# Optimization experiments

Measured on AMD Instinct MI355X. Metric: run time of the kernel, lower is better.

## Reference

```python
import jax, jax.numpy as jnp
import numpy as np

N_NODES = 50000


def gcn_conv(x, W, b, src, dst, n):
    # dense transform first (as PyG GCNConv does), then sparse aggregate
    h = x @ W  # [N, out]
    # add self loops
    loop = jnp.arange(n, dtype=src.dtype)
    s = jnp.concatenate([src, loop])
    d = jnp.concatenate([dst, loop])
    # symmetric normalization: deg over targets with unit edge weights
    deg = jax.ops.segment_sum(jnp.ones_like(d, dtype=h.dtype), d, num_segments=n)
    dinv = jnp.where(deg > 0, jax.lax.rsqrt(deg), 0.0)
    norm = dinv[s] * dinv[d]  # [E+N]
    msg = h[s] * norm[:, None]  # gather + scale
    out = jax.ops.segment_sum(msg, d, num_segments=n)  # scatter-add
    return out + b


def setup_inputs() -> dict:
    key = jax.random.key(0)
    k1, k2, k3, k4, k5 = jax.random.split(key, 5)
    in_dim, hid, out_dim = 256, 128, 16
    x = jax.random.normal(k1, (N_NODES, in_dim), dtype=jnp.float32)
    edge_index = jax.random.randint(k2, (2, 800000), 0, N_NODES, dtype=jnp.int64)
    # Glorot-style init for GCNConv weights, zero bias (PyG default)
    W1 = jax.random.normal(k3, (in_dim, hid), dtype=jnp.float32) / np.sqrt(in_dim)
    b1 = jnp.zeros((hid,), dtype=jnp.float32)
    W2 = jax.random.normal(k4, (hid, out_dim), dtype=jnp.float32) / np.sqrt(hid)
    b2 = jnp.zeros((out_dim,), dtype=jnp.float32)
    return {"x": x, "edge_index": edge_index, "W1": W1, "b1": b1, "W2": W2, "b2": b2}


def reference(x, edge_index, W1, b1, W2, b2):
    # eval-mode forward: dropout is identity
    src, dst = edge_index[0], edge_index[1]
    n = x.shape[0]
    h = gcn_conv(x, W1, b1, src, dst, n)
    h = jax.nn.relu(h)
    h = gcn_conv(h, W2, b2, src, dst, n)
    return jax.nn.log_softmax(h, axis=1)
```

## Files before the change

### kernel.cpp

```cpp
#include <hip/hip_runtime.h>
#include <hip/hip_bf16.h>

#define N_NODES 50000
#define E_EDGES 800000
#define IN_DIM  256
#define HID     128
#define OUT_DIM 16

#define NBUCK 391
#define NBLK  128
#define P2CAP 4096
#define GB1   391

using frag_ab = __attribute__((ext_vector_type(8))) short;
using frag_cd = __attribute__((ext_vector_type(4))) float;

static __device__ inline short f2bf(float f) {
    union { float f; unsigned u; } v; v.f = f;
    unsigned r = (v.u + 0x7fffu + ((v.u >> 16) & 1u)) >> 16;
    return (short)r;
}
static __device__ inline float bflo(unsigned u) {
    union { unsigned u; float f; } v; v.u = u << 16; return v.f;
}
static __device__ inline float bfhi(unsigned u) {
    union { unsigned u; float f; } v; v.u = u & 0xffff0000u; return v.f;
}
static __device__ inline unsigned packbf(float a, float b) {
    return (unsigned)(unsigned short)f2bf(a) | ((unsigned)(unsigned short)f2bf(b) << 16);
}

__global__ __launch_bounds__(512) void k1_gemm1_csra(const float* __restrict__ x,
                                                     const float* __restrict__ W1,
                                                     const int4* __restrict__ dst4,
                                                     const float* __restrict__ W2,
                                                     int* __restrict__ cnt_bb,
                                                     short* __restrict__ w2t,
                                                     short* __restrict__ h1s) {
    __shared__ uint4 lwt[64 * 64];
    int tid = threadIdx.x;

    if (blockIdx.x == GB1 + NBLK) {
        int n0 = tid >> 5, k0 = (tid & 31) * 4;
#pragma unroll
        for (int i = 0; i < 4; ++i)
            w2t[n0 * HID + k0 + i] = f2bf(W2[(k0 + i) * OUT_DIM + n0]);
        return;
    }
    if (blockIdx.x >= GB1) {
        int* hist = (int*)lwt;
        int bb = blockIdx.x - GB1;
        for (int i = tid; i < NBUCK; i += 512) hist[i] = 0;
        __syncthreads();
        for (int i = bb * 512 + tid; i < E_EDGES / 4; i += NBLK * 512) {
            int4 d = dst4[i];
            atomicAdd(&hist[d.x >> 7], 1);
            atomicAdd(&hist[d.y >> 7], 1);
            atomicAdd(&hist[d.z >> 7], 1);
            atomicAdd(&hist[d.w >> 7], 1);
        }
        __syncthreads();
        for (int i = tid; i < NBUCK; i += 512) cnt_bb[i * NBLK + bb] = hist[i];
        return;
    }

#pragma unroll
    for (int it = 0; it < 8; ++it) {
        int j = it * 512 + tid;
        int f = j >> 6, lane_ = j & 63;
        int kt = f >> 3, tt = f & 7;
        int mm = lane_ & 15, qq = lane_ >> 4;
        int c = tt * 16 + mm;
        int k0 = kt * 32 + qq * 8;
        unsigned p[4];
#pragma unroll
        for (int i = 0; i < 4; ++i)
            p[i] = packbf(W1[(k0 + 2 * i) * HID + c], W1[(k0 + 2 * i + 1) * HID + c]);
        uint4 v; v.x = p[0]; v.y = p[1]; v.z = p[2]; v.w = p[3];
        lwt[j] = v;
    }

    int wave = tid >> 6;
    int lane = tid & 63;
    int m = lane & 15;
    int q = lane >> 4;
    int row0 = blockIdx.x * 128 + wave * 16;
    int arow_idx = row0 + m;
    const float4* arow4 = (const float4*)(x + (size_t)(arow_idx < N_NODES ? arow_idx : 0) * IN_DIM);

    frag_ab a[8];
#pragma unroll
    for (int kt = 0; kt < 8; ++kt) {
        float4 f0 = arow4[kt * 8 + q * 2];
        float4 f1 = arow4[kt * 8 + q * 2 + 1];
        a[kt][0] = f2bf(f0.x); a[kt][1] = f2bf(f0.y); a[kt][2] = f2bf(f0.z); a[kt][3] = f2bf(f0.w);
        a[kt][4] = f2bf(f1.x); a[kt][5] = f2bf(f1.y); a[kt][6] = f2bf(f1.z); a[kt][7] = f2bf(f1.w);
    }

    frag_cd acc[8];
#pragma unroll
    for (int t = 0; t < 8; ++t) acc[t] = frag_cd{0.f, 0.f, 0.f, 0.f};

    __syncthreads();

#pragma unroll
    for (int kt = 0; kt < 8; ++kt) {
#pragma unroll
        for (int t = 0; t < 8; ++t) {
            frag_ab b = *(const frag_ab*)&lwt[(kt * 8 + t) * 64 + lane];
            acc[t] = __builtin_amdgcn_mfma_f32_16x16x32_bf16(a[kt], b, acc[t], 0, 0, 0);
        }
    }

#pragma unroll
    for (int t = 0; t < 8; ++t) {
#pragma unroll
        for (int r = 0; r < 4; ++r) {
            int orow = row0 + q * 4 + r;
            if (orow < N_NODES)
                h1s[(size_t)orow * HID + t * 16 + m] = f2bf(acc[t][r]);
        }
    }
}

__global__ __launch_bounds__(NBLK) void csr_b1(int* __restrict__ cnt_bb,
                                               int* __restrict__ btot) {
    __shared__ int sm[NBLK];
    int b = blockIdx.x, t = threadIdx.x;
    int v = cnt_bb[b * NBLK + t];
    sm[t] = v;
    __syncthreads();
    for (int o = 1; o < NBLK; o <<= 1) {
        int u = (t >= o) ? sm[t - o] : 0;
        __syncthreads();
        sm[t] += u;
        __syncthreads();
    }
    cnt_bb[b * NBLK + t] = sm[t] - v;
    if (t == NBLK - 1) btot[b] = sm[t];
}

__global__ __launch_bounds__(512) void csr_c2(const int4* __restrict__ src4,
                                              const int4* __restrict__ dst4,
                                              const int* __restrict__ cnt_bb,
                                              const int* __restrict__ btot,
                                              int* __restrict__ bbase,
                                              unsigned* __restrict__ tmp) {
    __shared__ int run[NBUCK];
    __shared__ int sc[512];
    int t = threadIdx.x;
    int v = (t < NBUCK) ? btot[t] : 0;
    sc[t] = v;
    __syncthreads();
    for (int o = 1; o < 512; o <<= 1) {
        int u = (t >= o) ? sc[t - o] : 0;
        __syncthreads();
        sc[t] += u;
        __syncthreads();
    }
    if (t < NBUCK) {
        int exc = sc[t] - v;
        run[t] = exc + cnt_bb[t * NBLK + blockIdx.x];
        if (blockIdx.x == 0) bbase[t] = exc;
    }
    if (blockIdx.x == 0 && t == 511) bbase[NBUCK] = sc[511];
    __syncthreads();
    for (int i = blockIdx.x * 512 + t; i < E_EDGES / 4; i += NBLK * 512) {
        int4 d = dst4[i];
        int4 s = src4[i];
        int p0 = atomicAdd(&run[d.x >> 7], 1);
        tmp[p0] = (unsigned)s.x | ((unsigned)(d.x & 127) << 17);
        int p1 = atomicAdd(&run[d.y >> 7], 1);
        tmp[p1] = (unsigned)s.y | ((unsigned)(d.y & 127) << 17);
        int p2 = atomicAdd(&run[d.z >> 7], 1);
        tmp[p2] = (unsigned)s.z | ((unsigned)(d.z & 127) << 17);
        int p3 = atomicAdd(&run[d.w >> 7], 1);
        tmp[p3] = (unsigned)s.w | ((unsigned)(d.w & 127) << 17);
    }
}

__global__ __launch_bounds__(256) void csr_p2s(const unsigned* __restrict__ tmp,
                                               const int* __restrict__ bbase,
                                               int* __restrict__ rowptr,
                                               float* __restrict__ dinv,
                                               int* __restrict__ ssrc,
                                               short* __restrict__ h1s) {
    __shared__ unsigned ed[P2CAP];
    __shared__ int cnt[128];
    __shared__ int off[128];
    __shared__ float sdv[128];
    int b = blockIdx.x, t = threadIdx.x;
    int base = bbase[b];
    int m = bbase[b + 1] - base;
    if (m > P2CAP) m = P2CAP;
    if (t < 128) cnt[t] = 0;
    __syncthreads();
    for (int i = t; i < m; i += 256) {
        unsigned v = tmp[base + i];
        ed[i] = v;
        atomicAdd(&cnt[v >> 17], 1);
    }
    __syncthreads();
    if (t < 128) off[t] = cnt[t];
    __syncthreads();
    for (int o = 1; o < 128; o <<= 1) {
        int u = (t >= o && t < 128) ? off[t - o] : 0;
        __syncthreads();
        if (t < 128) off[t] += u;
        __syncthreads();
    }
    if (t < 128) {
        int node = b * 128 + t;
        int ex = off[t] - cnt[t];
        float dv = rsqrtf((float)(cnt[t] + 1));
        sdv[t] = dv;
        if (node < N_NODES) {
            rowptr[node] = base + ex;
            dinv[node] = dv;
        }
        off[t] = ex;
    }
    if (b == NBUCK - 1 && t == 0) rowptr[N_NODES] = E_EDGES;
    __syncthreads();
    for (int i = t; i < m; i += 256) {
        unsigned v = ed[i];
        int p = atomicAdd(&off[v >> 17], 1);
        ssrc[base + p] = (int)(v & 0x1FFFF);
    }
    for (int idx = t; idx < 128 * 16; idx += 256) {
        int nl = idx >> 4;
        int wd = idx & 15;
        int node = b * 128 + nl;
        if (node < N_NODES) {
            uint4* p = (uint4*)(h1s + (size_t)node * HID) + wd;
            uint4 u = *p;
            float dv = sdv[nl];
            u.x = packbf(dv * bflo(u.x), dv * bfhi(u.x));
            u.y = packbf(dv * bflo(u.y), dv * bfhi(u.y));
            u.z = packbf(dv * bflo(u.z), dv * bfhi(u.z));
            u.w = packbf(dv * bflo(u.w), dv * bfhi(u.w));
            *p = u;
        }
    }
}

__global__ __launch_bounds__(256) void agg1_pull(const short* __restrict__ h1s,
                                                 const float* __restrict__ dinv,
                                                 const float* __restrict__ b1,
                                                 const int* __restrict__ rowptr,
                                                 const int* __restrict__ ssrc,
                                                 uint4* __restrict__ out1) {
    int wave = threadIdx.x >> 6;
    int lane = threadIdx.x & 63;
    int node = __builtin_amdgcn_readfirstlane(blockIdx.x * 4 + wave);
    if (node >= N_NODES) return;
    int eo = lane >> 4;
    int g  = lane & 15;

    int lo = rowptr[node], hi = rowptr[node + 1];
    float dd = dinv[node];
    float a0 = 0.f, a1 = 0.f, a2 = 0.f, a3 = 0.f;
    float a4 = 0.f, a5 = 0.f, a6 = 0.f, a7 = 0.f;

    if (eo == 0) {
        uint4 u = *(const uint4*)(h1s + (size_t)node * HID + g * 8);
        a0 = bflo(u.x); a1 = bfhi(u.x); a2 = bflo(u.y); a3 = bfhi(u.y);
        a4 = bflo(u.z); a5 = bfhi(u.z); a6 = bflo(u.w); a7 = bfhi(u.w);
    }

    int e = lo;
    for (; e + 16 <= hi; e += 16) {
        int s0 = ssrc[e + eo];
        int s1 = ssrc[e + 4 + eo];
        int s2 = ssrc[e + 8 + eo];
        int s3 = ssrc[e + 12 + eo];
        uint4 u0 = *(const uint4*)(h1s + (size_t)s0 * HID + g * 8);
        uint4 u1 = *(const uint4*)(h1s + (size_t)s1 * HID + g * 8);
        uint4 u2 = *(const uint4*)(h1s + (size_t)s2 * HID + g * 8);
        uint4 u3 = *(const uint4*)(h1s + (size_t)s3 * HID + g * 8);
        a0 += bflo(u0.x); a1 += bfhi(u0.x); a2 += bflo(u0.y); a3 += bfhi(u0.y);
        a4 += bflo(u0.z); a5 += bfhi(u0.z); a6 += bflo(u0.w); a7 += bfhi(u0.w);
        a0 += bflo(u1.x); a1 += bfhi(u1.x); a2 += bflo(u1.y); a3 += bfhi(u1.y);
        a4 += bflo(u1.z); a5 += bfhi(u1.z); a6 += bflo(u1.w); a7 += bfhi(u1.w);
        a0 += bflo(u2.x); a1 += bfhi(u2.x); a2 += bflo(u2.y); a3 += bfhi(u2.y);
        a4 += bflo(u2.z); a5 += bfhi(u2.z); a6 += bflo(u2.w); a7 += bfhi(u2.w);
        a0 += bflo(u3.x); a1 += bfhi(u3.x); a2 += bflo(u3.y); a3 += bfhi(u3.y);
        a4 += bflo(u3.z); a5 += bfhi(u3.z); a6 += bflo(u3.w); a7 += bfhi(u3.w);
    }
    for (; e + 4 <= hi; e += 4) {
        int s = ssrc[e + eo];
        uint4 u = *(const uint4*)(h1s + (size_t)s * HID + g * 8);
        a0 += bflo(u.x); a1 += bfhi(u.x); a2 += bflo(u.y); a3 += bfhi(u.y);
        a4 += bflo(u.z); a5 += bfhi(u.z); a6 += bflo(u.w); a7 += bfhi(u.w);
    }
    if (eo < hi - e) {
        int s = ssrc[e + eo];
        uint4 u = *(const uint4*)(h1s + (size_t)s * HID + g * 8);
        a0 += bflo(u.x); a1 += bfhi(u.x); a2 += bflo(u.y); a3 += bfhi(u.y);
        a4 += bflo(u.z); a5 += bfhi(u.z); a6 += bflo(u.w); a7 += bfhi(u.w);
    }

    a0 += __shfl_xor(a0, 16); a1 += __shfl_xor(a1, 16);
    a2 += __shfl_xor(a2, 16); a3 += __shfl_xor(a3, 16);
    a4 += __shfl_xor(a4, 16); a5 += __shfl_xor(a5, 16);
    a6 += __shfl_xor(a6, 16); a7 += __shfl_xor(a7, 16);
    a0 += __shfl_xor(a0, 32); a1 += __shfl_xor(a1, 32);
    a2 += __shfl_xor(a2, 32); a3 += __shfl_xor(a3, 32);
    a4 += __shfl_xor(a4, 32); a5 += __shfl_xor(a5, 32);
    a6 += __shfl_xor(a6, 32); a7 += __shfl_xor(a7, 32);

    if (eo == 0) {
        float4 bA = *(const float4*)(b1 + g * 8);
        float4 bB = *(const float4*)(b1 + g * 8 + 4);
        float o0 = fmaxf(fmaf(dd, a0, bA.x), 0.f);
        float o1 = fmaxf(fmaf(dd, a1, bA.y), 0.f);
        float o2 = fmaxf(fmaf(dd, a2, bA.z), 0.f);
        float o3 = fmaxf(fmaf(dd, a3, bA.w), 0.f);
        float o4 = fmaxf(fmaf(dd, a4, bB.x), 0.f);
        float o5 = fmaxf(fmaf(dd, a5, bB.y), 0.f);
        float o6 = fmaxf(fmaf(dd, a6, bB.z), 0.f);
        float o7 = fmaxf(fmaf(dd, a7, bB.w), 0.f);
        uint4 st;
        st.x = packbf(o0, o1); st.y = packbf(o2, o3);
        st.z = packbf(o4, o5); st.w = packbf(o6, o7);
        out1[(size_t)node * 16 + g] = st;
    }
}

__global__ __launch_bounds__(256) void gemm2_mfma(const short* __restrict__ out1,
                                                  const short* __restrict__ w2t,
                                                  const float* __restrict__ dinv,
                                                  short* __restrict__ h2s) {
    int wave = threadIdx.x >> 6;
    int lane = threadIdx.x & 63;
    int m = lane & 15;
    int q = lane >> 4;
    int row0 = blockIdx.x * 64 + wave * 16;
    int arow = row0 + m;
    if (arow >= N_NODES) arow = N_NODES - 1;
    const short* ap = out1 + (size_t)arow * HID + q * 8;
    const short* bp = w2t + m * HID + q * 8;

    frag_cd acc = frag_cd{0.f, 0.f, 0.f, 0.f};
#pragma unroll
    for (int kt = 0; kt < 4; ++kt) {
        frag_ab a = *(const frag_ab*)(ap + kt * 32);
        frag_ab b = *(const frag_ab*)(bp + kt * 32);
        acc = __builtin_amdgcn_mfma_f32_16x16x32_bf16(a, b, acc, 0, 0, 0);
    }
#pragma unroll
    for (int r = 0; r < 4; ++r) {
        int row = row0 + q * 4 + r;
        if (row < N_NODES)
            h2s[(size_t)row * OUT_DIM + m] = f2bf(acc[r] * dinv[row]);
    }
}

__global__ __launch_bounds__(256) void agg2_pull(const unsigned* __restrict__ h2s,
                                                 const float* __restrict__ dinv,
                                                 const float* __restrict__ b2,
                                                 const int* __restrict__ rowptr,
                                                 const int* __restrict__ ssrc,
                                                 float* __restrict__ out) {
    int wave = threadIdx.x >> 6;
    int lane = threadIdx.x & 63;
    int node = __builtin_amdgcn_readfirstlane(blockIdx.x * 4 + wave);
    if (node >= N_NODES) return;
    int eo = lane >> 3;
    int g  = lane & 7;

    int lo = rowptr[node], hi = rowptr[node + 1];
    float a0 = 0.f, a1 = 0.f;
    if (eo == 0) {
        unsigned u = h2s[(size_t)node * 8 + g];
        a0 = bflo(u); a1 = bfhi(u);
    }
    int e = lo;
    for (; e + 16 <= hi; e += 16) {
        int s0 = ssrc[e + eo];
        int s1 = ssrc[e + 8 + eo];
        unsigned u0 = h2s[(size_t)s0 * 8 + g];
        unsigned u1 = h2s[(size_t)s1 * 8 + g];
        a0 += bflo(u0); a1 += bfhi(u0);
        a0 += bflo(u1); a1 += bfhi(u1);
    }
    for (; e + 8 <= hi; e += 8) {
        int s = ssrc[e + eo];
        unsigned u = h2s[(size_t)s * 8 + g];
        a0 += bflo(u); a1 += bfhi(u);
    }
    if (eo < hi - e) {
        int s = ssrc[e + eo];
        unsigned u = h2s[(size_t)s * 8 + g];
        a0 += bflo(u); a1 += bfhi(u);
    }

    a0 += __shfl_xor(a0, 8);  a1 += __shfl_xor(a1, 8);
    a0 += __shfl_xor(a0, 16); a1 += __shfl_xor(a1, 16);
    a0 += __shfl_xor(a0, 32); a1 += __shfl_xor(a1, 32);

    float dd = dinv[node];
    float2 bb = *(const float2*)(b2 + 2 * g);
    float v0 = fmaf(dd, a0, bb.x);
    float v1 = fmaf(dd, a1, bb.y);

    float m = fmaxf(v0, v1);
#pragma unroll
    for (int msk = 1; msk < 8; msk <<= 1) m = fmaxf(m, __shfl_xor(m, msk));
    float s2 = __expf(v0 - m) + __expf(v1 - m);
#pragma unroll
    for (int msk = 1; msk < 8; msk <<= 1) s2 += __shfl_xor(s2, msk);
    float lse = m + __logf(s2);
    if (eo == 0) {
        float2 o; o.x = v0 - lse; o.y = v1 - lse;
        *(float2*)(out + (size_t)node * OUT_DIM + 2 * g) = o;
    }
}

extern "C" void kernel_launch(void* const* d_in, const int* in_sizes, int n_in,
                              void* d_out, int out_size, void* d_ws, size_t ws_size,
                              hipStream_t stream) {
    const float* x  = (const float*)d_in[0];
    const int*   ei = (const int*)d_in[1];
    const float* W1 = (const float*)d_in[2];
    const float* b1 = (const float*)d_in[3];
    const float* W2 = (const float*)d_in[4];
    const float* b2 = (const float*)d_in[5];
    float* out = (float*)d_out;

    const int n = N_NODES;
    const int e = E_EDGES;
    const int* srcp = ei;
    const int* dstp = ei + e;

    char* w = (char*)d_ws;
    int*      cnt_bb = (int*)w;        w += (size_t)NBUCK * NBLK * 4;
    int*      btot   = (int*)w;        w += (size_t)NBUCK * 4;
    int*      bbase  = (int*)w;        w += (size_t)(NBUCK + 1) * 4;
    int*      rowptr = (int*)w;        w += (size_t)(n + 1) * 4;
    float*    dinv   = (float*)w;      w += (size_t)n * 4;
    unsigned* tmp    = (unsigned*)w;   w += (size_t)e * 4;
    int*      ssrc   = (int*)w;        w += (size_t)e * 4;
    short*    w2t    = (short*)w;      w += (size_t)OUT_DIM * HID * 2;
    short*    h1s    = (short*)w;      w += (size_t)n * HID * 2;
    short*    out1   = (short*)w;      w += (size_t)n * HID * 2;
    short*    h2s    = (short*)w;      w += (size_t)n * OUT_DIM * 2;

    auto blk = [](long long total, int b) { return (int)((total + b - 1) / b); };

    k1_gemm1_csra<<<GB1 + NBLK + 1, 512, 0, stream>>>(x, W1, (const int4*)dstp, W2,
                                                      cnt_bb, w2t, h1s);
    csr_b1<<<NBUCK, NBLK, 0, stream>>>(cnt_bb, btot);
    csr_c2<<<NBLK, 512, 0, stream>>>((const int4*)srcp, (const int4*)dstp,
                                     cnt_bb, btot, bbase, tmp);
    csr_p2s<<<NBUCK, 256, 0, stream>>>(tmp, bbase, rowptr, dinv, ssrc, h1s);
    agg1_pull<<<blk(n, 4), 256, 0, stream>>>(h1s, dinv, b1, rowptr, ssrc, (uint4*)out1);
    gemm2_mfma<<<blk(n, 64), 256, 0, stream>>>(out1, w2t, dinv, h2s);
    agg2_pull<<<blk(n, 4), 256, 0, stream>>>((const unsigned*)h2s, dinv, b2,
                                             rowptr, ssrc, out);
}
```

Before: 189.6 us.

## Fuse layer-2 GEMM into aggregation and merge bucket scan into scatter kernel

The separate csr_b1 scan kernel is removed. Each csr_c2b block now computes its per-bucket totals and prefix directly from cnt_bb rows. The agg1 kernel now multiplies the ReLU'd aggregated row by W2 in fp32 using shuffles, so out1 is never written and gemm2 is gone. This drops two launches and an N×128 bf16 round trip to memory. In exchange, each csr block redundantly reads the whole cnt_bb matrix, and agg1 does extra FMA and shuffle work per node.

New measurement: 213.4 us. +12.6%, slower.

```diff
diff --git a/kernel.cpp b/kernel.cpp
--- a/kernel.cpp
+++ b/kernel.cpp
@@ -33,20 +33,11 @@
 __global__ __launch_bounds__(512) void k1_gemm1_csra(const float* __restrict__ x,
                                                      const float* __restrict__ W1,
                                                      const int4* __restrict__ dst4,
-                                                     const float* __restrict__ W2,
                                                      int* __restrict__ cnt_bb,
-                                                     short* __restrict__ w2t,
                                                      short* __restrict__ h1s) {
     __shared__ uint4 lwt[64 * 64];
     int tid = threadIdx.x;
 
-    if (blockIdx.x == GB1 + NBLK) {
-        int n0 = tid >> 5, k0 = (tid & 31) * 4;
-#pragma unroll
-        for (int i = 0; i < 4; ++i)
-            w2t[n0 * HID + k0 + i] = f2bf(W2[(k0 + i) * OUT_DIM + n0]);
-        return;
-    }
     if (blockIdx.x >= GB1) {
         int* hist = (int*)lwt;
         int bb = blockIdx.x - GB1;
@@ -123,34 +114,28 @@
     }
 }
 
-__global__ __launch_bounds__(NBLK) void csr_b1(int* __restrict__ cnt_bb,
-                                               int* __restrict__ btot) {
-    __shared__ int sm[NBLK];
-    int b = blockIdx.x, t = threadIdx.x;
-    int v = cnt_bb[b * NBLK + t];
-    sm[t] = v;
-    __syncthreads();
-    for (int o = 1; o < NBLK; o <<= 1) {
-        int u = (t >= o) ? sm[t - o] : 0;
-        __syncthreads();
-        sm[t] += u;
-        __syncthreads();
-    }
-    cnt_bb[b * NBLK + t] = sm[t] - v;
-    if (t == NBLK - 1) btot[b] = sm[t];
-}
-
-__global__ __launch_bounds__(512) void csr_c2(const int4* __restrict__ src4,
-                                              const int4* __restrict__ dst4,
-                                              const int* __restrict__ cnt_bb,
-                                              const int* __restrict__ btot,
-                                              int* __restrict__ bbase,
-                                              unsigned* __restrict__ tmp) {
+__global__ __launch_bounds__(512) void csr_c2b(const int4* __restrict__ src4,
+                                               const int4* __restrict__ dst4,
+                                               const int* __restrict__ cnt_bb,
+                                               int* __restrict__ bbase,
+                                               unsigned* __restrict__ tmp) {
     __shared__ int run[NBUCK];
     __shared__ int sc[512];
     int t = threadIdx.x;
-    int v = (t < NBUCK) ? btot[t] : 0;
-    sc[t] = v;
+    int j = blockIdx.x;
+    int tot = 0, pre = 0;
+    if (t < NBUCK) {
+        const int4* row = (const int4*)(cnt_bb + t * NBLK);
+#pragma unroll 4
+        for (int b4 = 0; b4 < NBLK / 4; ++b4) {
+            int4 c = row[b4];
+            int b = b4 * 4;
+            tot += c.x + c.y + c.z + c.w;
+            pre += (b + 0 < j ? c.x : 0) + (b + 1 < j ? c.y : 0)
+                 + (b + 2 < j ? c.z : 0) + (b + 3 < j ? c.w : 0);
+        }
+    }
+    sc[t] = tot;
     __syncthreads();
     for (int o = 1; o < 512; o <<= 1) {
         int u = (t >= o) ? sc[t - o] : 0;
@@ -159,13 +144,13 @@
         __syncthreads();
     }
     if (t < NBUCK) {
-        int exc = sc[t] - v;
-        run[t] = exc + cnt_bb[t * NBLK + blockIdx.x];
-        if (blockIdx.x == 0) bbase[t] = exc;
-    }
-    if (blockIdx.x == 0 && t == 511) bbase[NBUCK] = sc[511];
-    __syncthreads();
-    for (int i = blockIdx.x * 512 + t; i < E_EDGES / 4; i += NBLK * 512) {
+        int exc = sc[t] - tot;
+        run[t] = exc + pre;
+        if (j == 0) bbase[t] = exc;
+    }
+    if (j == 0 && t == 511) bbase[NBUCK] = sc[511];
+    __syncthreads();
+    for (int i = j * 512 + t; i < E_EDGES / 4; i += NBLK * 512) {
         int4 d = dst4[i];
         int4 s = src4[i];
         int p0 = atomicAdd(&run[d.x >> 7], 1);
@@ -244,12 +229,13 @@
     }
 }
 
-__global__ __launch_bounds__(256) void agg1_pull(const short* __restrict__ h1s,
-                                                 const float* __restrict__ dinv,
-                                                 const float* __restrict__ b1,
-                                                 const int* __restrict__ rowptr,
-                                                 const int* __restrict__ ssrc,
-                                                 uint4* __restrict__ out1) {
+__global__ __launch_bounds__(256) void agg1_w2(const short* __restrict__ h1s,
+                                               const float* __restrict__ dinv,
+                                               const float* __restrict__ b1,
+                                               const float* __restrict__ W2,
+                                               const int* __restrict__ rowptr,
+                                               const int* __restrict__ ssrc,
+                                               short* __restrict__ h2s) {
     int wave = threadIdx.x >> 6;
     int lane = threadIdx.x & 63;
     int node = __builtin_amdgcn_readfirstlane(blockIdx.x * 4 + wave);
@@ -309,50 +295,37 @@
     a4 += __shfl_xor(a4, 32); a5 += __shfl_xor(a5, 32);
     a6 += __shfl_xor(a6, 32); a7 += __shfl_xor(a7, 32);
 
-    if (eo == 0) {
-        float4 bA = *(const float4*)(b1 + g * 8);
-        float4 bB = *(const float4*)(b1 + g * 8 + 4);
-        float o0 = fmaxf(fmaf(dd, a0, bA.x), 0.f);
-        float o1 = fmaxf(fmaf(dd, a1, bA.y), 0.f);
-        float o2 = fmaxf(fmaf(dd, a2, bA.z), 0.f);
-        float o3 = fmaxf(fmaf(dd, a3, bA.w), 0.f);
-        float o4 = fmaxf(fmaf(dd, a4, bB.x), 0.f);
-        float o5 = fmaxf(fmaf(dd, a5, bB.y), 0.f);
-        float o6 = fmaxf(fmaf(dd, a6, bB.z), 0.f);
-        float o7 = fmaxf(fmaf(dd, a7, bB.w), 0.f);
-        uint4 st;
-        st.x = packbf(o0, o1); st.y = packbf(o2, o3);
-        st.z = packbf(o4, o5); st.w = packbf(o6, o7);
-        out1[(size_t)node * 16 + g] = st;
-    }
-}
-
-__global__ __launch_bounds__(256) void gemm2_mfma(const short* __restrict__ out1,
-                                                  const short* __restrict__ w2t,
-                                                  const float* __restrict__ dinv,
-                                                  short* __restrict__ h2s) {
-    int wave = threadIdx.x >> 6;
-    int lane = threadIdx.x & 63;
-    int m = lane & 15;
-    int q = lane >> 4;
-    int row0 = blockIdx.x * 64 + wave * 16;
-    int arow = row0 + m;
-    if (arow >= N_NODES) arow = N_NODES - 1;
-    const short* ap = out1 + (size_t)arow * HID + q * 8;
-    const short* bp = w2t + m * HID + q * 8;
-
-    frag_cd acc = frag_cd{0.f, 0.f, 0.f, 0.f};
-#pragma unroll
-    for (int kt = 0; kt < 4; ++kt) {
-        frag_ab a = *(const frag_ab*)(ap + kt * 32);
-        frag_ab b = *(const frag_ab*)(bp + kt * 32);
-        acc = __builtin_amdgcn_mfma_f32_16x16x32_bf16(a, b, acc, 0, 0, 0);
-    }
-#pragma unroll
-    for (int r = 0; r < 4; ++r) {
-        int row = row0 + q * 4 + r;
-        if (row < N_NODES)
-            h2s[(size_t)row * OUT_DIM + m] = f2bf(acc[r] * dinv[row]);
+    float4 bA = *(const float4*)(b1 + g * 8);
+    float4 bB = *(const float4*)(b1 + g * 8 + 4);
+    float vv[8];
+    vv[0] = fmaxf(fmaf(dd, a0, bA.x), 0.f);
+    vv[1] = fmaxf(fmaf(dd, a1, bA.y), 0.f);
+    vv[2] = fmaxf(fmaf(dd, a2, bA.z), 0.f);
+    vv[3] = fmaxf(fmaf(dd, a3, bA.w), 0.f);
+    vv[4] = fmaxf(fmaf(dd, a4, bB.x), 0.f);
+    vv[5] = fmaxf(fmaf(dd, a5, bB.y), 0.f);
+    vv[6] = fmaxf(fmaf(dd, a6, bB.z), 0.f);
+    vv[7] = fmaxf(fmaf(dd, a7, bB.w), 0.f);
+
+    float p0 = 0.f, p1 = 0.f, p2 = 0.f, p3 = 0.f;
+#pragma unroll
+    for (int i = 0; i < 8; ++i) {
+        float4 w2r = *(const float4*)(W2 + (g * 8 + i) * OUT_DIM + eo * 4);
+        p0 = fmaf(vv[i], w2r.x, p0);
+        p1 = fmaf(vv[i], w2r.y, p1);
+        p2 = fmaf(vv[i], w2r.z, p2);
+        p3 = fmaf(vv[i], w2r.w, p3);
+    }
+#pragma unroll
+    for (int msk = 1; msk <= 8; msk <<= 1) {
+        p0 += __shfl_xor(p0, msk); p1 += __shfl_xor(p1, msk);
+        p2 += __shfl_xor(p2, msk); p3 += __shfl_xor(p3, msk);
+    }
+    if (g == 0) {
+        uint2 st;
+        st.x = packbf(p0 * dd, p1 * dd);
+        st.y = packbf(p2 * dd, p3 * dd);
+        *(uint2*)(h2s + (size_t)node * OUT_DIM + eo * 4) = st;
     }
 }
 
@@ -435,27 +408,21 @@
 
     char* w = (char*)d_ws;
     int*      cnt_bb = (int*)w;        w += (size_t)NBUCK * NBLK * 4;
-    int*      btot   = (int*)w;        w += (size_t)NBUCK * 4;
     int*      bbase  = (int*)w;        w += (size_t)(NBUCK + 1) * 4;
     int*      rowptr = (int*)w;        w += (size_t)(n + 1) * 4;
     float*    dinv   = (float*)w;      w += (size_t)n * 4;
     unsigned* tmp    = (unsigned*)w;   w += (size_t)e * 4;
     int*      ssrc   = (int*)w;        w += (size_t)e * 4;
-    short*    w2t    = (short*)w;      w += (size_t)OUT_DIM * HID * 2;
     short*    h1s    = (short*)w;      w += (size_t)n * HID * 2;
-    short*    out1   = (short*)w;      w += (size_t)n * HID * 2;
     short*    h2s    = (short*)w;      w += (size_t)n * OUT_DIM * 2;
 
     auto blk = [](long long total, int b) { return (int)((total + b - 1) / b); };
 
-    k1_gemm1_csra<<<GB1 + NBLK + 1, 512, 0, stream>>>(x, W1, (const int4*)dstp, W2,
-                                                      cnt_bb, w2t, h1s);
-    csr_b1<<<NBUCK, NBLK, 0, stream>>>(cnt_bb, btot);
-    csr_c2<<<NBLK, 512, 0, stream>>>((const int4*)srcp, (const int4*)dstp,
-                                     cnt_bb, btot, bbase, tmp);
+    k1_gemm1_csra<<<GB1 + NBLK, 512, 0, stream>>>(x, W1, (const int4*)dstp, cnt_bb, h1s);
+    csr_c2b<<<NBLK, 512, 0, stream>>>((const int4*)srcp, (const int4*)dstp,
+                                      cnt_bb, bbase, tmp);
     csr_p2s<<<NBUCK, 256, 0, stream>>>(tmp, bbase, rowptr, dinv, ssrc, h1s);
-    agg1_pull<<<blk(n, 4), 256, 0, stream>>>(h1s, dinv, b1, rowptr, ssrc, (uint4*)out1);
-    gemm2_mfma<<<blk(n, 64), 256, 0, stream>>>(out1, w2t, dinv, h2s);
+    agg1_w2<<<blk(n, 4), 256, 0, stream>>>(h1s, dinv, b1, W2, rowptr, ssrc, h2s);
     agg2_pull<<<blk(n, 4), 256, 0, stream>>>((const unsigned*)h2s, dinv, b2,
                                              rowptr, ssrc, out);
 }
```

## Fold degree normalization into GEMM1 epilogue via early global degree histogram

Applied to the files above, without the earlier changes.

Computes per-node in-degree with global atomics in a new first kernel alongside the bucket histogram. GEMM1 then applies the rsqrt-degree scale in its epilogue and writes dinv, so the separate read-modify-write pass over h1s in the CSR sort kernel is removed. The bucket prefix-scan is merged into the GEMM launch, dropping one kernel. The cost is 800k global atomics, an extra memset, and the GEMM no longer overlapping with the histogram in a single launch.

New measurement: 222.7 us. 1.17x slower.

```diff
diff --git a/kernel.cpp b/kernel.cpp
--- a/kernel.cpp
+++ b/kernel.cpp
@@ -30,37 +30,62 @@
     return (unsigned)(unsigned short)f2bf(a) | ((unsigned)(unsigned short)f2bf(b) << 16);
 }
 
-__global__ __launch_bounds__(512) void k1_gemm1_csra(const float* __restrict__ x,
-                                                     const float* __restrict__ W1,
-                                                     const int4* __restrict__ dst4,
-                                                     const float* __restrict__ W2,
-                                                     int* __restrict__ cnt_bb,
-                                                     short* __restrict__ w2t,
-                                                     short* __restrict__ h1s) {
-    __shared__ uint4 lwt[64 * 64];
+__global__ __launch_bounds__(512) void k1_csra_deg(const int4* __restrict__ dst4,
+                                                   const float* __restrict__ W2,
+                                                   int* __restrict__ cnt_bb,
+                                                   int* __restrict__ deg,
+                                                   short* __restrict__ w2t) {
     int tid = threadIdx.x;
-
-    if (blockIdx.x == GB1 + NBLK) {
+    if (blockIdx.x == NBLK) {
         int n0 = tid >> 5, k0 = (tid & 31) * 4;
 #pragma unroll
         for (int i = 0; i < 4; ++i)
             w2t[n0 * HID + k0 + i] = f2bf(W2[(k0 + i) * OUT_DIM + n0]);
         return;
     }
+    __shared__ int hist[NBUCK];
+    int bb = blockIdx.x;
+    for (int i = tid; i < NBUCK; i += 512) hist[i] = 0;
+    __syncthreads();
+    for (int i = bb * 512 + tid; i < E_EDGES / 4; i += NBLK * 512) {
+        int4 d = dst4[i];
+        atomicAdd(&hist[d.x >> 7], 1);
+        atomicAdd(&hist[d.y >> 7], 1);
+        atomicAdd(&hist[d.z >> 7], 1);
+        atomicAdd(&hist[d.w >> 7], 1);
+        atomicAdd(&deg[d.x], 1);
+        atomicAdd(&deg[d.y], 1);
+        atomicAdd(&deg[d.z], 1);
+        atomicAdd(&deg[d.w], 1);
+    }
+    __syncthreads();
+    for (int i = tid; i < NBUCK; i += 512) cnt_bb[i * NBLK + bb] = hist[i];
+}
+
+__global__ __launch_bounds__(512) void k2_gemm1_b1(const float* __restrict__ x,
+                                                   const float* __restrict__ W1,
+                                                   const int* __restrict__ deg,
+                                                   int* __restrict__ cnt_bb,
+                                                   int* __restrict__ btot,
+                                                   float* __restrict__ dinv,
+                                                   short* __restrict__ h1s) {
+    __shared__ uint4 lwt[64 * 64];
+    int tid = threadIdx.x;
+
     if (blockIdx.x >= GB1) {
-        int* hist = (int*)lwt;
-        int bb = blockIdx.x - GB1;
-        for (int i = tid; i < NBUCK; i += 512) hist[i] = 0;
+        int* sm = (int*)lwt;
+        int b = blockIdx.x - GB1, t = tid;
+        int v = 0;
+        if (t < NBLK) { v = cnt_bb[b * NBLK + t]; sm[t] = v; }
         __syncthreads();
-        for (int i = bb * 512 + tid; i < E_EDGES / 4; i += NBLK * 512) {
-            int4 d = dst4[i];
-            atomicAdd(&hist[d.x >> 7], 1);
-            atomicAdd(&hist[d.y >> 7], 1);
-            atomicAdd(&hist[d.z >> 7], 1);
-            atomicAdd(&hist[d.w >> 7], 1);
+        for (int o = 1; o < NBLK; o <<= 1) {
+            int u = (t >= o && t < NBLK) ? sm[t - o] : 0;
+            __syncthreads();
+            if (t < NBLK) sm[t] += u;
+            __syncthreads();
         }
-        __syncthreads();
-        for (int i = tid; i < NBUCK; i += 512) cnt_bb[i * NBLK + bb] = hist[i];
+        if (t < NBLK) cnt_bb[b * NBLK + t] = sm[t] - v;
+        if (t == NBLK - 1) btot[b] = sm[t];
         return;
     }
 
@@ -112,32 +137,28 @@
         }
     }
 
+    float dv[4];
+#pragma unroll
+    for (int r = 0; r < 4; ++r) {
+        int orow = row0 + q * 4 + r;
+        dv[r] = (orow < N_NODES) ? rsqrtf((float)(deg[orow] + 1)) : 0.f;
+    }
+    if (m == 0) {
+#pragma unroll
+        for (int r = 0; r < 4; ++r) {
+            int orow = row0 + q * 4 + r;
+            if (orow < N_NODES) dinv[orow] = dv[r];
+        }
+    }
 #pragma unroll
     for (int t = 0; t < 8; ++t) {
 #pragma unroll
         for (int r = 0; r < 4; ++r) {
             int orow = row0 + q * 4 + r;
             if (orow < N_NODES)
-                h1s[(size_t)orow * HID + t * 16 + m] = f2bf(acc[t][r]);
+                h1s[(size_t)orow * HID + t * 16 + m] = f2bf(acc[t][r] * dv[r]);
         }
     }
-}
-
-__global__ __launch_bounds__(NBLK) void csr_b1(int* __restrict__ cnt_bb,
-                                               int* __restrict__ btot) {
-    __shared__ int sm[NBLK];
-    int b = blockIdx.x, t = threadIdx.x;
-    int v = cnt_bb[b * NBLK + t];
-    sm[t] = v;
-    __syncthreads();
-    for (int o = 1; o < NBLK; o <<= 1) {
-        int u = (t >= o) ? sm[t - o] : 0;
-        __syncthreads();
-        sm[t] += u;
-        __syncthreads();
-    }
-    cnt_bb[b * NBLK + t] = sm[t] - v;
-    if (t == NBLK - 1) btot[b] = sm[t];
 }
 
 __global__ __launch_bounds__(512) void csr_c2(const int4* __restrict__ src4,
@@ -179,16 +200,13 @@
     }
 }
 
-__global__ __launch_bounds__(256) void csr_p2s(const unsigned* __restrict__ tmp,
-                                               const int* __restrict__ bbase,
-                                               int* __restrict__ rowptr,
-                                               float* __restrict__ dinv,
-                                               int* __restrict__ ssrc,
-                                               short* __restrict__ h1s) {
+__global__ __launch_bounds__(256) void csr_p2(const unsigned* __restrict__ tmp,
+                                              const int* __restrict__ bbase,
+                                              int* __restrict__ rowptr,
+                                              int* __restrict__ ssrc) {
     __shared__ unsigned ed[P2CAP];
     __shared__ int cnt[128];
     __shared__ int off[128];
-    __shared__ float sdv[128];
     int b = blockIdx.x, t = threadIdx.x;
     int base = bbase[b];
     int m = bbase[b + 1] - base;
@@ -212,12 +230,7 @@
     if (t < 128) {
         int node = b * 128 + t;
         int ex = off[t] - cnt[t];
-        float dv = rsqrtf((float)(cnt[t] + 1));
-        sdv[t] = dv;
-        if (node < N_NODES) {
-            rowptr[node] = base + ex;
-            dinv[node] = dv;
-        }
+        if (node < N_NODES) rowptr[node] = base + ex;
         off[t] = ex;
     }
     if (b == NBUCK - 1 && t == 0) rowptr[N_NODES] = E_EDGES;
@@ -226,21 +239,6 @@
         unsigned v = ed[i];
         int p = atomicAdd(&off[v >> 17], 1);
         ssrc[base + p] = (int)(v & 0x1FFFF);
-    }
-    for (int idx = t; idx < 128 * 16; idx += 256) {
-        int nl = idx >> 4;
-        int wd = idx & 15;
-        int node = b * 128 + nl;
-        if (node < N_NODES) {
-            uint4* p = (uint4*)(h1s + (size_t)node * HID) + wd;
-            uint4 u = *p;
-            float dv = sdv[nl];
-            u.x = packbf(dv * bflo(u.x), dv * bfhi(u.x));
-            u.y = packbf(dv * bflo(u.y), dv * bfhi(u.y));
-            u.z = packbf(dv * bflo(u.z), dv * bfhi(u.z));
-            u.w = packbf(dv * bflo(u.w), dv * bfhi(u.w));
-            *p = u;
-        }
     }
 }
 
@@ -437,6 +435,7 @@
     int*      cnt_bb = (int*)w;        w += (size_t)NBUCK * NBLK * 4;
     int*      btot   = (int*)w;        w += (size_t)NBUCK * 4;
     int*      bbase  = (int*)w;        w += (size_t)(NBUCK + 1) * 4;
+    int*      deg    = (int*)w;        w += (size_t)n * 4;
     int*      rowptr = (int*)w;        w += (size_t)(n + 1) * 4;
     float*    dinv   = (float*)w;      w += (size_t)n * 4;
     unsigned* tmp    = (unsigned*)w;   w += (size_t)e * 4;
@@ -448,12 +447,12 @@
 
     auto blk = [](long long total, int b) { return (int)((total + b - 1) / b); };
 
-    k1_gemm1_csra<<<GB1 + NBLK + 1, 512, 0, stream>>>(x, W1, (const int4*)dstp, W2,
-                                                      cnt_bb, w2t, h1s);
-    csr_b1<<<NBUCK, NBLK, 0, stream>>>(cnt_bb, btot);
+    hipMemsetAsync(deg, 0, (size_t)n * sizeof(int), stream);
+    k1_csra_deg<<<NBLK + 1, 512, 0, stream>>>((const int4*)dstp, W2, cnt_bb, deg, w2t);
+    k2_gemm1_b1<<<GB1 + NBUCK, 512, 0, stream>>>(x, W1, deg, cnt_bb, btot, dinv, h1s);
     csr_c2<<<NBLK, 512, 0, stream>>>((const int4*)srcp, (const int4*)dstp,
                                      cnt_bb, btot, bbase, tmp);
-    csr_p2s<<<NBUCK, 256, 0, stream>>>(tmp, bbase, rowptr, dinv, ssrc, h1s);
+    csr_p2<<<NBUCK, 256, 0, stream>>>(tmp, bbase, rowptr, ssrc);
     agg1_pull<<<blk(n, 4), 256, 0, stream>>>(h1s, dinv, b1, rowptr, ssrc, (uint4*)out1);
     gemm2_mfma<<<blk(n, 64), 256, 0, stream>>>(out1, w2t, dinv, h2s);
     agg2_pull<<<blk(n, 4), 256, 0, stream>>>((const unsigned*)h2s, dinv, b2,
```

## Fold bucket prefix scan into scatter kernel and move degree scaling earlier

Applied to the files above, without the earlier changes.

Removes the separate per-bucket scan kernel: each scatter block now recomputes bucket totals and its own prefix directly from the count matrix. Node degrees are counted with global atomics during the histogram pass, so dinv and the h1 prescaling can run in extra blocks of the scatter kernel instead of in the final CSR pass. This drops one kernel launch and takes the scaling pass off the critical tail. In exchange it adds 800K global atomics, a memset, and redundant reads of the count matrix in every scatter block.

Measured after the change: 217.1 us. 14.5% more time.

```diff
diff --git a/kernel.cpp b/kernel.cpp
--- a/kernel.cpp
+++ b/kernel.cpp
@@ -11,6 +11,7 @@
 #define NBLK  128
 #define P2CAP 4096
 #define GB1   391
+#define NCHUNK 98
 
 using frag_ab = __attribute__((ext_vector_type(8))) short;
 using frag_cd = __attribute__((ext_vector_type(4))) float;
@@ -35,6 +36,7 @@
                                                      const int4* __restrict__ dst4,
                                                      const float* __restrict__ W2,
                                                      int* __restrict__ cnt_bb,
+                                                     int* __restrict__ deg,
                                                      short* __restrict__ w2t,
                                                      short* __restrict__ h1s) {
     __shared__ uint4 lwt[64 * 64];
@@ -58,6 +60,10 @@
             atomicAdd(&hist[d.y >> 7], 1);
             atomicAdd(&hist[d.z >> 7], 1);
             atomicAdd(&hist[d.w >> 7], 1);
+            atomicAdd(&deg[d.x], 1);
+            atomicAdd(&deg[d.y], 1);
+            atomicAdd(&deg[d.z], 1);
+            atomicAdd(&deg[d.w], 1);
         }
         __syncthreads();
         for (int i = tid; i < NBUCK; i += 512) cnt_bb[i * NBLK + bb] = hist[i];
@@ -123,34 +129,51 @@
     }
 }
 
-__global__ __launch_bounds__(NBLK) void csr_b1(int* __restrict__ cnt_bb,
-                                               int* __restrict__ btot) {
-    __shared__ int sm[NBLK];
-    int b = blockIdx.x, t = threadIdx.x;
-    int v = cnt_bb[b * NBLK + t];
-    sm[t] = v;
-    __syncthreads();
-    for (int o = 1; o < NBLK; o <<= 1) {
-        int u = (t >= o) ? sm[t - o] : 0;
-        __syncthreads();
-        sm[t] += u;
-        __syncthreads();
-    }
-    cnt_bb[b * NBLK + t] = sm[t] - v;
-    if (t == NBLK - 1) btot[b] = sm[t];
-}
-
-__global__ __launch_bounds__(512) void csr_c2(const int4* __restrict__ src4,
-                                              const int4* __restrict__ dst4,
-                                              const int* __restrict__ cnt_bb,
-                                              const int* __restrict__ btot,
-                                              int* __restrict__ bbase,
-                                              unsigned* __restrict__ tmp) {
+__global__ __launch_bounds__(512) void k2_scatter_scale(const int4* __restrict__ src4,
+                                                        const int4* __restrict__ dst4,
+                                                        const int* __restrict__ cnt_bb,
+                                                        const int* __restrict__ deg,
+                                                        int* __restrict__ bbase,
+                                                        float* __restrict__ dinv,
+                                                        short* __restrict__ h1s,
+                                                        unsigned* __restrict__ tmp) {
+    int t = threadIdx.x;
+    if (blockIdx.x >= NBLK) {
+        int base_node = (blockIdx.x - NBLK) * 512;
+        for (int idx = t; idx < 512 * 16; idx += 512) {
+            int nl = idx >> 4;
+            int wd = idx & 15;
+            int node = base_node + nl;
+            if (node < N_NODES) {
+                float dv = rsqrtf((float)(deg[node] + 1));
+                if (wd == 0) dinv[node] = dv;
+                uint4* p = (uint4*)(h1s + (size_t)node * HID) + wd;
+                uint4 u = *p;
+                u.x = packbf(dv * bflo(u.x), dv * bfhi(u.x));
+                u.y = packbf(dv * bflo(u.y), dv * bfhi(u.y));
+                u.z = packbf(dv * bflo(u.z), dv * bfhi(u.z));
+                u.w = packbf(dv * bflo(u.w), dv * bfhi(u.w));
+                *p = u;
+            }
+        }
+        return;
+    }
     __shared__ int run[NBUCK];
     __shared__ int sc[512];
-    int t = threadIdx.x;
-    int v = (t < NBUCK) ? btot[t] : 0;
-    sc[t] = v;
+    int j = blockIdx.x;
+    int tot = 0, pre = 0;
+    if (t < NBUCK) {
+        const int4* row = (const int4*)(cnt_bb + t * NBLK);
+#pragma unroll 4
+        for (int b4 = 0; b4 < NBLK / 4; ++b4) {
+            int4 c = row[b4];
+            int b = b4 * 4;
+            tot += c.x + c.y + c.z + c.w;
+            pre += (b + 0 < j ? c.x : 0) + (b + 1 < j ? c.y : 0)
+                 + (b + 2 < j ? c.z : 0) + (b + 3 < j ? c.w : 0);
+        }
+    }
+    sc[t] = tot;
     __syncthreads();
     for (int o = 1; o < 512; o <<= 1) {
         int u = (t >= o) ? sc[t - o] : 0;
@@ -159,13 +182,13 @@
         __syncthreads();
     }
     if (t < NBUCK) {
-        int exc = sc[t] - v;
-        run[t] = exc + cnt_bb[t * NBLK + blockIdx.x];
-        if (blockIdx.x == 0) bbase[t] = exc;
-    }
-    if (blockIdx.x == 0 && t == 511) bbase[NBUCK] = sc[511];
-    __syncthreads();
-    for (int i = blockIdx.x * 512 + t; i < E_EDGES / 4; i += NBLK * 512) {
+        int exc = sc[t] - tot;
+        run[t] = exc + pre;
+        if (j == 0) bbase[t] = exc;
+    }
+    if (j == 0 && t == 511) bbase[NBUCK] = sc[511];
+    __syncthreads();
+    for (int i = j * 512 + t; i < E_EDGES / 4; i += NBLK * 512) {
         int4 d = dst4[i];
         int4 s = src4[i];
         int p0 = atomicAdd(&run[d.x >> 7], 1);
@@ -179,16 +202,13 @@
     }
 }
 
-__global__ __launch_bounds__(256) void csr_p2s(const unsigned* __restrict__ tmp,
-                                               const int* __restrict__ bbase,
-                                               int* __restrict__ rowptr,
-                                               float* __restrict__ dinv,
-                                               int* __restrict__ ssrc,
-                                               short* __restrict__ h1s) {
+__global__ __launch_bounds__(256) void csr_p2(const unsigned* __restrict__ tmp,
+                                              const int* __restrict__ bbase,
+                                              int* __restrict__ rowptr,
+                                              int* __restrict__ ssrc) {
     __shared__ unsigned ed[P2CAP];
     __shared__ int cnt[128];
     __shared__ int off[128];
-    __shared__ float sdv[128];
     int b = blockIdx.x, t = threadIdx.x;
     int base = bbase[b];
     int m = bbase[b + 1] - base;
@@ -212,12 +232,7 @@
     if (t < 128) {
         int node = b * 128 + t;
         int ex = off[t] - cnt[t];
-        float dv = rsqrtf((float)(cnt[t] + 1));
-        sdv[t] = dv;
-        if (node < N_NODES) {
-            rowptr[node] = base + ex;
-            dinv[node] = dv;
-        }
+        if (node < N_NODES) rowptr[node] = base + ex;
         off[t] = ex;
     }
     if (b == NBUCK - 1 && t == 0) rowptr[N_NODES] = E_EDGES;
@@ -226,21 +241,6 @@
         unsigned v = ed[i];
         int p = atomicAdd(&off[v >> 17], 1);
         ssrc[base + p] = (int)(v & 0x1FFFF);
-    }
-    for (int idx = t; idx < 128 * 16; idx += 256) {
-        int nl = idx >> 4;
-        int wd = idx & 15;
-        int node = b * 128 + nl;
-        if (node < N_NODES) {
-            uint4* p = (uint4*)(h1s + (size_t)node * HID) + wd;
-            uint4 u = *p;
-            float dv = sdv[nl];
-            u.x = packbf(dv * bflo(u.x), dv * bfhi(u.x));
-            u.y = packbf(dv * bflo(u.y), dv * bfhi(u.y));
-            u.z = packbf(dv * bflo(u.z), dv * bfhi(u.z));
-            u.w = packbf(dv * bflo(u.w), dv * bfhi(u.w));
-            *p = u;
-        }
     }
 }
 
@@ -435,8 +435,8 @@
 
     char* w = (char*)d_ws;
     int*      cnt_bb = (int*)w;        w += (size_t)NBUCK * NBLK * 4;
-    int*      btot   = (int*)w;        w += (size_t)NBUCK * 4;
     int*      bbase  = (int*)w;        w += (size_t)(NBUCK + 1) * 4;
+    int*      deg    = (int*)w;        w += (size_t)n * 4;
     int*      rowptr = (int*)w;        w += (size_t)(n + 1) * 4;
     float*    dinv   = (float*)w;      w += (size_t)n * 4;
     unsigned* tmp    = (unsigned*)w;   w += (size_t)e * 4;
@@ -448,12 +448,14 @@
 
     auto blk = [](long long total, int b) { return (int)((total + b - 1) / b); };
 
+    hipMemsetAsync(deg, 0, (size_t)n * sizeof(int), stream);
     k1_gemm1_csra<<<GB1 + NBLK + 1, 512, 0, stream>>>(x, W1, (const int4*)dstp, W2,
-                                                      cnt_bb, w2t, h1s);
-    csr_b1<<<NBUCK, NBLK, 0, stream>>>(cnt_bb, btot);
-    csr_c2<<<NBLK, 512, 0, stream>>>((const int4*)srcp, (const int4*)dstp,
-                                     cnt_bb, btot, bbase, tmp);
-    csr_p2s<<<NBUCK, 256, 0, stream>>>(tmp, bbase, rowptr, dinv, ssrc, h1s);
+                                                      cnt_bb, deg, w2t, h1s);
+    k2_scatter_scale<<<NBLK + NCHUNK, 512, 0, stream>>>((const int4*)srcp,
+                                                        (const int4*)dstp,
+                                                        cnt_bb, deg, bbase,
+                                                        dinv, h1s, tmp);
+    csr_p2<<<NBUCK, 256, 0, stream>>>(tmp, bbase, rowptr, ssrc);
     agg1_pull<<<blk(n, 4), 256, 0, stream>>>(h1s, dinv, b1, rowptr, ssrc, (uint4*)out1);
     gemm2_mfma<<<blk(n, 64), 256, 0, stream>>>(out1, w2t, dinv, h2s);
     agg2_pull<<<blk(n, 4), 256, 0, stream>>>((const unsigned*)h2s, dinv, b2,
```
